# Performance work log

Hardware: AMD Instinct MI355X
Metric: run time of the kernel (lower is better)

The kernel has to match this reference:

```python
import jax, jax.numpy as jnp
import numpy as np

B, H, W, D = 8, 32, 32, 384      # batch, height, width, channels (=dim)
E, HID, O = 8, 1536, 384         # num_experts, mlp hidden (dim*4), out_dim
TOP_K = 2


def setup_inputs() -> dict:
    key = jax.random.key(0)
    ks = jax.random.split(key, 5)
    x = jax.random.normal(ks[0], (B, H, W, D), dtype=jnp.float32)
    # router (noise_linear unused: eval path, train=False)
    Wg = 0.02 * jax.random.normal(ks[1], (D, E), dtype=jnp.float32)
    bg = jnp.zeros((E,), dtype=jnp.float32)
    # per-expert MLP params stacked along expert axis
    W1 = 0.02 * jax.random.normal(ks[2], (E, D, HID), dtype=jnp.float32)
    b1 = jnp.zeros((E, HID), dtype=jnp.float32)
    W2 = 0.02 * jax.random.normal(ks[3], (E, HID, O), dtype=jnp.float32)
    b2 = jnp.zeros((E, O), dtype=jnp.float32)
    return {"x": x, "Wg": Wg, "bg": bg, "W1": W1, "b1": b1, "W2": W2, "b2": b2}


def reference(x, Wg, bg, W1, b1, W2, b2):
    # --- NoisyTopkRouter (eval: train=False -> no noise branch) ---
    logits = jnp.einsum('bhwd,de->bhwe', x, Wg) + bg            # [B,H,W,E]
    _, top_idx = jax.lax.top_k(logits, TOP_K)                   # [B,H,W,K]
    # mask of selected experts; sparse logits = logits where selected, -inf else
    sel = jnp.sum(jax.nn.one_hot(top_idx, E, dtype=jnp.float32), axis=-2) > 0
    sparse_logits = jnp.where(sel, logits, -jnp.inf)
    gates = jax.nn.softmax(sparse_logits, axis=-1)              # zero on non-top-k

    # --- experts: since gate is exactly 0 off the top-k, the masked
    # gather-MLP-scatter loop equals a gate-weighted sum of all expert MLPs ---
    h = jnp.einsum('bhwd,edf->bhwef', x, W1) + b1               # [B,H,W,E,HID]
    h = jax.nn.gelu(h, approximate=False)                       # torch nn.GELU = exact
    y = jnp.einsum('bhwef,efo->bhweo', h, W2) + b2              # [B,H,W,E,O]
    out = jnp.einsum('bhweo,bhwe->bhwo', y, gates)              # [B,H,W,O]
    return out
```

## Files before the change

### kernel.cpp

```cpp
#include <hip/hip_runtime.h>
#include <cmath>

#define N_TOK 8192
#define DIM   384
#define NEXP  8
#define HID   1536
#define OUTD  384
#define CAP_MT 72
#define CAP_TOK 2304
#define CAP_TB 18

typedef __attribute__((ext_vector_type(8)))  __bf16 bf16x8;
typedef __attribute__((ext_vector_type(16))) float  f32x16;
typedef __attribute__((ext_vector_type(4)))  float  f32x4;
typedef __attribute__((ext_vector_type(8)))  unsigned short u16x8;

__device__ __forceinline__ unsigned short f2bf(float f) {
    unsigned u = __float_as_uint(f);
    u += 0x7FFF + ((u >> 16) & 1);
    return (unsigned short)(u >> 16);
}

__device__ __forceinline__ float bf2f(unsigned short s) {
    return __uint_as_float(((unsigned)s) << 16);
}

__device__ __forceinline__ float gelu_exact(float x) {
    return 0.5f * x * (1.0f + erff(x * 0.70710678118654752f));
}

__device__ __forceinline__ void cp16(const unsigned short* g, unsigned short* l) {
    __builtin_amdgcn_global_load_lds(
        (const __attribute__((address_space(1))) unsigned int*)g,
        (__attribute__((address_space(3))) unsigned int*)l, 16, 0, 0);
}

__global__ void swizzle_kernel(const float* __restrict__ W1, const float* __restrict__ W2,
                               unsigned short* __restrict__ w1s, unsigned short* __restrict__ w2s,
                               int* __restrict__ cnt) {
    if (blockIdx.x == 0 && threadIdx.x < NEXP) cnt[threadIdx.x] = 0;
    int gid = blockIdx.x * blockDim.x + threadIdx.x;
    const int T1 = NEXP * 48 * 24 * 64;
    const int T2 = NEXP * 12 * 96 * 64;
    const float* src; unsigned short* dst; int K, N, NT, KT, g;
    if (gid < T1)           { src = W1; dst = w1s; K = DIM; N = HID;  NT = 48; KT = 24; g = gid; }
    else if (gid < T1 + T2) { src = W2; dst = w2s; K = HID; N = OUTD; NT = 12; KT = 96; g = gid - T1; }
    else return;
    int l  = g & 63;
    int kt = (g >> 6) % KT;
    int nt = ((g >> 6) / KT) % NT;
    int e  = g / (64 * KT * NT);
    const float* s = src + ((size_t)e * K + kt * 16 + (l >> 5) * 8) * N + nt * 32 + (l & 31);
    unsigned short r[8];
    #pragma unroll
    for (int j = 0; j < 8; ++j) r[j] = f2bf(s[(size_t)j * N]);
    *(uint4*)(dst + (size_t)g * 8) = *(uint4*)r;
}

__global__ void router_kernel(const float* __restrict__ x, const float* __restrict__ Wg,
                              const float* __restrict__ bg, int* __restrict__ cnt,
                              int* __restrict__ btok, int* __restrict__ tokmap,
                              float* __restrict__ gmap) {
    __shared__ float WgL[NEXP * DIM];
    __shared__ int lcnt[NEXP];
    __shared__ int lbase[NEXP];
    int tid = threadIdx.x;
    for (int i = tid; i < DIM * NEXP; i += 256) {
        int ch = i >> 3, e = i & 7;
        WgL[e * DIM + ch] = Wg[i];
    }
    if (tid < NEXP) lcnt[tid] = 0;
    __syncthreads();

    int tl  = tid >> 3;
    int seg = tid & 7;
    int t   = blockIdx.x * 32 + tl;

    float lg[NEXP] = {0.f, 0.f, 0.f, 0.f, 0.f, 0.f, 0.f, 0.f};
    const float* xr = x + (size_t)t * DIM;
    #pragma unroll
    for (int d4 = 0; d4 < 12; ++d4) {
        float4 v = *(const float4*)(xr + d4 * 32 + seg * 4);
        #pragma unroll
        for (int e = 0; e < NEXP; ++e) {
            float4 w = *(const float4*)&WgL[e * DIM + d4 * 32 + seg * 4];
            lg[e] += v.x * w.x + v.y * w.y + v.z * w.z + v.w * w.w;
        }
    }
    #pragma unroll
    for (int off = 1; off < 8; off <<= 1)
        #pragma unroll
        for (int e = 0; e < NEXP; ++e)
            lg[e] += __shfl_xor(lg[e], off);

    int p0 = 0, p1 = 0, i0 = 0, i1 = 0;
    float g0 = 0.f, g1 = 0.f;
    if (seg == 0) {
        float v0 = -INFINITY, v1 = -INFINITY;
        #pragma unroll
        for (int e = 0; e < NEXP; ++e) {
            float v = lg[e] + bg[e];
            if (v > v0)      { v1 = v0; i1 = i0; v0 = v; i0 = e; }
            else if (v > v1) { v1 = v;  i1 = e; }
        }
        float e1 = expf(v1 - v0);
        g0 = 1.f / (1.f + e1);
        g1 = e1  / (1.f + e1);
        p0 = atomicAdd(&lcnt[i0], 1);
        p1 = atomicAdd(&lcnt[i1], 1);
    }
    __syncthreads();
    if (tid < NEXP) lbase[tid] = atomicAdd(&cnt[tid], lcnt[tid]);
    __syncthreads();
    if (seg == 0) {
        int o0 = lbase[i0] + p0, o1 = lbase[i1] + p1;
        btok[i0 * N_TOK + o0] = t;
        btok[i1 * N_TOK + o1] = t;
        ((int4*)tokmap)[t] = make_int4(i0, o0, i1, o1);
        ((float2*)gmap)[t] = make_float2(g0, g1);
    }
}

__global__ void gather_kernel(const float* __restrict__ x, const int* __restrict__ cnt,
                              const int* __restrict__ btok, unsigned short* __restrict__ xg) {
    int mt = blockIdx.x, e = blockIdx.y;
    int cntE = cnt[e];
    if (mt * 32 >= cntE) return;
    int tid = threadIdx.x;
    int m = tid & 31, kt0 = tid >> 5;
    int pos = mt * 32 + m;
    int idx = (pos < cntE) ? pos : cntE - 1;
    int tok = btok[e * N_TOK + idx];
    const float* xr = x + (size_t)tok * DIM;
    #pragma unroll
    for (int kk = 0; kk < 3; ++kk) {
        int kt = kt0 + kk * 8;
        #pragma unroll
        for (int kh = 0; kh < 2; ++kh) {
            float4 v0 = *(const float4*)(xr + kt * 16 + kh * 8);
            float4 v1 = *(const float4*)(xr + kt * 16 + kh * 8 + 4);
            unsigned short rr[8];
            rr[0] = f2bf(v0.x); rr[1] = f2bf(v0.y); rr[2] = f2bf(v0.z); rr[3] = f2bf(v0.w);
            rr[4] = f2bf(v1.x); rr[5] = f2bf(v1.y); rr[6] = f2bf(v1.z); rr[7] = f2bf(v1.w);
            *(uint4*)(xg + (size_t)(((e * CAP_MT + mt) * 24 + kt) * 64 + kh * 32 + m) * 8) =
                *(uint4*)rr;
        }
    }
}

__global__ __launch_bounds__(512, 4) void gemm1_kernel(
        const unsigned short* __restrict__ xg, const unsigned short* __restrict__ w1s,
        const float* __restrict__ b1, const int* __restrict__ cnt,
        unsigned short* __restrict__ h) {
    int L = blockIdx.x;
    int e = L & 7;
    int r = L >> 3;
    int nb = r % 12;
    int tb = r / 12;
    int cntE = cnt[e];
    if (tb * 128 >= cntE) return;

    __shared__ unsigned short stg[2][16384];

    int tid = threadIdx.x;
    int wave = tid >> 6, lane = tid & 63;
    int m31 = lane & 31, kh = lane >> 5;
    int wm = wave & 1;
    int wn = wave >> 1;

    f32x16 acc[2];
    acc[0] = (f32x16){0.f,0.f,0.f,0.f,0.f,0.f,0.f,0.f,0.f,0.f,0.f,0.f,0.f,0.f,0.f,0.f};
    acc[1] = acc[0];

    const unsigned short* xa = xg  + ((size_t)(e * CAP_MT + tb * 4) * 24) * 512;
    const unsigned short* wb = w1s + ((size_t)(e * 48 + nb * 4) * 24) * 512;

    const unsigned short* sbase = (wave < 4)
        ? xa + ((size_t)wave * 24) * 512 + lane * 8
        : wb + ((size_t)(wave - 4) * 24) * 512 + lane * 8;
    int tbase = (wave < 4) ? wave * 4 : 16 + (wave - 4) * 4;

    auto issue = [&](int ks) {
        unsigned short* dst = &stg[ks & 1][tbase * 512];
        const unsigned short* sk = sbase + (size_t)ks * 2048;
        #pragma unroll
        for (int q = 0; q < 4; ++q)
            cp16(sk + q * 512, dst + q * 512);
    };

    issue(0);
    for (int ks = 0; ks < 6; ++ks) {
        __syncthreads();
        if (ks < 5) issue(ks + 1);
        const unsigned short* bufp = stg[ks & 1];
        #pragma unroll
        for (int kt = 0; kt < 4; ++kt) {
            bf16x8 b  = *(const bf16x8*)&bufp[(16 + wn * 4 + kt) * 512 + lane * 8];
            bf16x8 a0 = *(const bf16x8*)&bufp[((wm * 2 + 0) * 4 + kt) * 512 + lane * 8];
            bf16x8 a1 = *(const bf16x8*)&bufp[((wm * 2 + 1) * 4 + kt) * 512 + lane * 8];
            acc[0] = __builtin_amdgcn_mfma_f32_32x32x16_bf16(a0, b, acc[0], 0, 0, 0);
            acc[1] = __builtin_amdgcn_mfma_f32_32x32x16_bf16(a1, b, acc[1], 0, 0, 0);
        }
    }

    __syncthreads();
    char* hw = (char*)stg + wave * 5120;
    float bv = b1[e * HID + nb * 128 + wn * 32 + m31];
    #pragma unroll
    for (int s = 0; s < 2; ++s)
        #pragma unroll
        for (int rr = 0; rr < 16; ++rr) {
            int rowl = s * 32 + (rr & 3) + 8 * (rr >> 2) + 4 * kh;
            *(unsigned short*)(hw + rowl * 80 + m31 * 2) = f2bf(gelu_exact(acc[s][rr] + bv));
        }
    #pragma unroll
    for (int mtl = 0; mtl < 2; ++mtl)
        #pragma unroll
        for (int ktl = 0; ktl < 2; ++ktl) {
            uint4 v = *(const uint4*)(hw + (mtl * 32 + m31) * 80 + (ktl * 16 + kh * 8) * 2);
            int mt = tb * 4 + wm * 2 + mtl;
            int kt = nb * 8 + wn * 2 + ktl;
            *(uint4*)(h + ((size_t)((e * CAP_MT + mt) * 96 + kt)) * 512 + lane * 8) = v;
        }
}

__global__ __launch_bounds__(512, 4) void gemm2_kernel(
        const unsigned short* __restrict__ h, const unsigned short* __restrict__ w2s,
        const int* __restrict__ cnt, unsigned short* __restrict__ yp) {
    int L = blockIdx.x;
    int e = L & 7;
    int r = L >> 3;
    int nb = r % 3;
    int tb = r / 3;
    int cntE = cnt[e];
    if (tb * 128 >= cntE) return;

    __shared__ unsigned short stg[2][16384];

    int tid = threadIdx.x;
    int wave = tid >> 6, lane = tid & 63;
    int m31 = lane & 31, kh = lane >> 5;
    int wm = wave & 1;
    int wn = wave >> 1;

    f32x16 acc[2];
    acc[0] = (f32x16){0.f,0.f,0.f,0.f,0.f,0.f,0.f,0.f,0.f,0.f,0.f,0.f,0.f,0.f,0.f,0.f};
    acc[1] = acc[0];

    const unsigned short* xa = h   + ((size_t)(e * CAP_MT + tb * 4) * 96) * 512;
    const unsigned short* wb = w2s + ((size_t)(e * 12 + nb * 4) * 96) * 512;

    const unsigned short* sbase = (wave < 4)
        ? xa + ((size_t)wave * 96) * 512 + lane * 8
        : wb + ((size_t)(wave - 4) * 96) * 512 + lane * 8;
    int tbase = (wave < 4) ? wave * 4 : 16 + (wave - 4) * 4;

    auto issue = [&](int ks) {
        unsigned short* dst = &stg[ks & 1][tbase * 512];
        const unsigned short* sk = sbase + (size_t)ks * 2048;
        #pragma unroll
        for (int q = 0; q < 4; ++q)
            cp16(sk + q * 512, dst + q * 512);
    };

    issue(0);
    for (int ks = 0; ks < 24; ++ks) {
        __syncthreads();
        if (ks < 23) issue(ks + 1);
        const unsigned short* bufp = stg[ks & 1];
        #pragma unroll
        for (int kt = 0; kt < 4; ++kt) {
            bf16x8 b  = *(const bf16x8*)&bufp[(16 + wn * 4 + kt) * 512 + lane * 8];
            bf16x8 a0 = *(const bf16x8*)&bufp[((wm * 2 + 0) * 4 + kt) * 512 + lane * 8];
            bf16x8 a1 = *(const bf16x8*)&bufp[((wm * 2 + 1) * 4 + kt) * 512 + lane * 8];
            acc[0] = __builtin_amdgcn_mfma_f32_32x32x16_bf16(a0, b, acc[0], 0, 0, 0);
            acc[1] = __builtin_amdgcn_mfma_f32_32x32x16_bf16(a1, b, acc[1], 0, 0, 0);
        }
    }

    __syncthreads();
    char* hw = (char*)stg + wave * 4096;
    #pragma unroll
    for (int s = 0; s < 2; ++s)
        #pragma unroll
        for (int rr = 0; rr < 16; ++rr) {
            int rowl = s * 32 + (rr & 3) + 8 * (rr >> 2) + 4 * kh;
            *(unsigned short*)(hw + rowl * 64 + m31 * 2) = f2bf(acc[s][rr]);
        }
    #pragma unroll
    for (int it = 0; it < 4; ++it) {
        int rowl = it * 16 + (lane >> 2);
        int cc   = lane & 3;
        uint4 v = *(const uint4*)(hw + rowl * 64 + cc * 16);
        int pos = tb * 128 + wm * 64 + rowl;
        *(uint4*)(yp + (size_t)(e * CAP_TOK + pos) * OUTD + nb * 128 + wn * 32 + cc * 8) = v;
    }
}

__global__ void reduce_kernel(const unsigned short* __restrict__ yp,
                              const int* __restrict__ tokmap, const float* __restrict__ gmap,
                              const float* __restrict__ b2, float* __restrict__ out) {
    int gid = blockIdx.x * 256 + threadIdx.x;
    int t = gid / 48, q = gid - t * 48;
    int4   tm = ((const int4*)tokmap)[t];
    float2 g  = ((const float2*)gmap)[t];
    const unsigned short* p0 = yp + ((size_t)(tm.x * CAP_TOK + tm.y)) * OUTD + q * 8;
    const unsigned short* p1 = yp + ((size_t)(tm.z * CAP_TOK + tm.w)) * OUTD + q * 8;
    u16x8 a = __builtin_nontemporal_load((const u16x8*)p0);
    u16x8 b = __builtin_nontemporal_load((const u16x8*)p1);
    const float* c0 = &b2[tm.x * OUTD + q * 8];
    const float* c1 = &b2[tm.z * OUTD + q * 8];
    f32x4 r0, r1;
    #pragma unroll
    for (int j = 0; j < 4; ++j) {
        r0[j] = g.x * (bf2f(a[j]) + c0[j]) + g.y * (bf2f(b[j]) + c1[j]);
        r1[j] = g.x * (bf2f(a[4 + j]) + c0[4 + j]) + g.y * (bf2f(b[4 + j]) + c1[4 + j]);
    }
    float* op = &out[(size_t)t * OUTD + q * 8];
    __builtin_nontemporal_store(r0, (f32x4*)op);
    __builtin_nontemporal_store(r1, (f32x4*)(op + 4));
}

extern "C" void kernel_launch(void* const* d_in, const int* in_sizes, int n_in,
                              void* d_out, int out_size, void* d_ws, size_t ws_size,
                              hipStream_t stream) {
    const float* x  = (const float*)d_in[0];
    const float* Wg = (const float*)d_in[1];
    const float* bg = (const float*)d_in[2];
    const float* W1 = (const float*)d_in[3];
    const float* b1 = (const float*)d_in[4];
    const float* W2 = (const float*)d_in[5];
    const float* b2 = (const float*)d_in[6];
    float* out = (float*)d_out;

    char* ws = (char*)d_ws;
    int*            cnt    = (int*)ws;
    int*            btok   = (int*)(ws + 1024);
    int*            tokmap = (int*)(ws + 263168);
    float*          gmap   = (float*)(ws + 394240);
    unsigned short* xg     = (unsigned short*)(ws + 459776);
    unsigned short* w1s    = (unsigned short*)(ws + 14615552);
    unsigned short* w2s    = (unsigned short*)(ws + 24052736);
    unsigned short* h      = (unsigned short*)(ws + 33489920);
    unsigned short* yp     = xg;

    hipLaunchKernelGGL(swizzle_kernel, dim3(4608), dim3(256), 0, stream,
                       W1, W2, w1s, w2s, cnt);
    hipLaunchKernelGGL(router_kernel, dim3(N_TOK / 32), dim3(256), 0, stream,
                       x, Wg, bg, cnt, btok, tokmap, gmap);
    hipLaunchKernelGGL(gather_kernel, dim3(CAP_MT, NEXP), dim3(256), 0, stream,
                       x, cnt, btok, xg);
    hipLaunchKernelGGL(gemm1_kernel, dim3(NEXP * 12 * CAP_TB), dim3(512), 0, stream,
                       xg, w1s, b1, cnt, h);
    hipLaunchKernelGGL(gemm2_kernel, dim3(NEXP * 3 * CAP_TB), dim3(512), 0, stream,
                       h, w2s, cnt, yp);
    hipLaunchKernelGGL(reduce_kernel, dim3(N_TOK * 48 / 256), dim3(256), 0, stream,
                       yp, tokmap, gmap, b2, out);
}
```

Baseline: 186.5 us.

## Switch expert GEMMs to triple-buffered LDS pipeline with explicit vmcnt waits

```diff
diff --git a/kernel.cpp b/kernel.cpp
--- a/kernel.cpp
+++ b/kernel.cpp
@@ -160,7 +160,7 @@
     int cntE = cnt[e];
     if (tb * 128 >= cntE) return;
 
-    __shared__ unsigned short stg[2][16384];
+    __shared__ unsigned short stg[3][12288];
 
     int tid = threadIdx.x;
     int wave = tid >> 6, lane = tid & 63;
@@ -178,30 +178,41 @@
     const unsigned short* sbase = (wave < 4)
         ? xa + ((size_t)wave * 24) * 512 + lane * 8
         : wb + ((size_t)(wave - 4) * 24) * 512 + lane * 8;
-    int tbase = (wave < 4) ? wave * 4 : 16 + (wave - 4) * 4;
+    int tbase = (wave < 4) ? wave * 3 : 12 + (wave - 4) * 3;
 
     auto issue = [&](int ks) {
-        unsigned short* dst = &stg[ks & 1][tbase * 512];
-        const unsigned short* sk = sbase + (size_t)ks * 2048;
-        #pragma unroll
-        for (int q = 0; q < 4; ++q)
+        unsigned short* dst = &stg[ks % 3][tbase * 512];
+        const unsigned short* sk = sbase + (size_t)ks * 1536;
+        #pragma unroll
+        for (int q = 0; q < 3; ++q)
             cp16(sk + q * 512, dst + q * 512);
     };
-
-    issue(0);
-    for (int ks = 0; ks < 6; ++ks) {
-        __syncthreads();
-        if (ks < 5) issue(ks + 1);
-        const unsigned short* bufp = stg[ks & 1];
-        #pragma unroll
-        for (int kt = 0; kt < 4; ++kt) {
-            bf16x8 b  = *(const bf16x8*)&bufp[(16 + wn * 4 + kt) * 512 + lane * 8];
-            bf16x8 a0 = *(const bf16x8*)&bufp[((wm * 2 + 0) * 4 + kt) * 512 + lane * 8];
-            bf16x8 a1 = *(const bf16x8*)&bufp[((wm * 2 + 1) * 4 + kt) * 512 + lane * 8];
+    auto consume = [&](int ks) {
+        const unsigned short* bufp = stg[ks % 3];
+        #pragma unroll
+        for (int kt = 0; kt < 3; ++kt) {
+            bf16x8 b  = *(const bf16x8*)&bufp[(12 + wn * 3 + kt) * 512 + lane * 8];
+            bf16x8 a0 = *(const bf16x8*)&bufp[((wm * 2 + 0) * 3 + kt) * 512 + lane * 8];
+            bf16x8 a1 = *(const bf16x8*)&bufp[((wm * 2 + 1) * 3 + kt) * 512 + lane * 8];
             acc[0] = __builtin_amdgcn_mfma_f32_32x32x16_bf16(a0, b, acc[0], 0, 0, 0);
             acc[1] = __builtin_amdgcn_mfma_f32_32x32x16_bf16(a1, b, acc[1], 0, 0, 0);
         }
-    }
+    };
+
+    issue(0); issue(1);
+    for (int ks = 0; ks < 7; ++ks) {
+        asm volatile("s_waitcnt vmcnt(3) lgkmcnt(0)" ::: "memory");
+        __builtin_amdgcn_sched_barrier(0);
+        __builtin_amdgcn_s_barrier();
+        __builtin_amdgcn_sched_barrier(0);
+        if (ks + 2 < 8) issue(ks + 2);
+        consume(ks);
+    }
+    asm volatile("s_waitcnt vmcnt(0) lgkmcnt(0)" ::: "memory");
+    __builtin_amdgcn_sched_barrier(0);
+    __builtin_amdgcn_s_barrier();
+    __builtin_amdgcn_sched_barrier(0);
+    consume(7);
 
     __syncthreads();
     char* hw = (char*)stg + wave * 5120;
@@ -235,7 +246,7 @@
     int cntE = cnt[e];
     if (tb * 128 >= cntE) return;
 
-    __shared__ unsigned short stg[2][16384];
+    __shared__ unsigned short stg[3][12288];
 
     int tid = threadIdx.x;
     int wave = tid >> 6, lane = tid & 63;
@@ -253,30 +264,41 @@
     const unsigned short* sbase = (wave < 4)
         ? xa + ((size_t)wave * 96) * 512 + lane * 8
         : wb + ((size_t)(wave - 4) * 96) * 512 + lane * 8;
-    int tbase = (wave < 4) ? wave * 4 : 16 + (wave - 4) * 4;
+    int tbase = (wave < 4) ? wave * 3 : 12 + (wave - 4) * 3;
 
     auto issue = [&](int ks) {
-        unsigned short* dst = &stg[ks & 1][tbase * 512];
-        const unsigned short* sk = sbase + (size_t)ks * 2048;
-        #pragma unroll
-        for (int q = 0; q < 4; ++q)
+        unsigned short* dst = &stg[ks % 3][tbase * 512];
+        const unsigned short* sk = sbase + (size_t)ks * 1536;
+        #pragma unroll
+        for (int q = 0; q < 3; ++q)
             cp16(sk + q * 512, dst + q * 512);
     };
-
-    issue(0);
-    for (int ks = 0; ks < 24; ++ks) {
-        __syncthreads();
-        if (ks < 23) issue(ks + 1);
-        const unsigned short* bufp = stg[ks & 1];
-        #pragma unroll
-        for (int kt = 0; kt < 4; ++kt) {
-            bf16x8 b  = *(const bf16x8*)&bufp[(16 + wn * 4 + kt) * 512 + lane * 8];
-            bf16x8 a0 = *(const bf16x8*)&bufp[((wm * 2 + 0) * 4 + kt) * 512 + lane * 8];
-            bf16x8 a1 = *(const bf16x8*)&bufp[((wm * 2 + 1) * 4 + kt) * 512 + lane * 8];
+    auto consume = [&](int ks) {
+        const unsigned short* bufp = stg[ks % 3];
+        #pragma unroll
+        for (int kt = 0; kt < 3; ++kt) {
+            bf16x8 b  = *(const bf16x8*)&bufp[(12 + wn * 3 + kt) * 512 + lane * 8];
+            bf16x8 a0 = *(const bf16x8*)&bufp[((wm * 2 + 0) * 3 + kt) * 512 + lane * 8];
+            bf16x8 a1 = *(const bf16x8*)&bufp[((wm * 2 + 1) * 3 + kt) * 512 + lane * 8];
             acc[0] = __builtin_amdgcn_mfma_f32_32x32x16_bf16(a0, b, acc[0], 0, 0, 0);
             acc[1] = __builtin_amdgcn_mfma_f32_32x32x16_bf16(a1, b, acc[1], 0, 0, 0);
         }
-    }
+    };
+
+    issue(0); issue(1);
+    for (int ks = 0; ks < 31; ++ks) {
+        asm volatile("s_waitcnt vmcnt(3) lgkmcnt(0)" ::: "memory");
+        __builtin_amdgcn_sched_barrier(0);
+        __builtin_amdgcn_s_barrier();
+        __builtin_amdgcn_sched_barrier(0);
+        if (ks + 2 < 32) issue(ks + 2);
+        consume(ks);
+    }
+    asm volatile("s_waitcnt vmcnt(0) lgkmcnt(0)" ::: "memory");
+    __builtin_amdgcn_sched_barrier(0);
+    __builtin_amdgcn_s_barrier();
+    __builtin_amdgcn_sched_barrier(0);
+    consume(31);
 
     __syncthreads();
     char* hw = (char*)stg + wave * 4096;
```

After: 183.8 us. Within noise of the previous version (-1.5%).
